# Performance work log

Measured on AMD Instinct MI355X. Metric: run time of the kernel, lower is better.

Reference implementation:

```python
import jax, jax.numpy as jnp
import numpy as np

STRIDES = (8, 4, 2, 1)
EPS = 1e-12  # F.normalize default eps


def _l2norm(x):
    return x / jnp.maximum(jnp.linalg.norm(x, axis=-1, keepdims=True), EPS)


def _stage(residual, stride, iw, ib, ow, ob, cb):
    B, D, T = residual.shape
    # avg_pool1d(stride, stride)
    zp = residual.reshape(B, D, T // stride, stride).mean(-1) if stride > 1 else residual
    # in_proj: 1x1 conv  [B,D,Ts] -> [B,C,Ts]
    z_e = jnp.einsum('bdt,cd->bct', zp, iw) + ib[None, :, None]
    C = z_e.shape[1]
    enc = z_e.transpose(0, 2, 1).reshape(-1, C)           # (B*Ts, C)
    enc_n = _l2norm(enc)
    cb_n = _l2norm(cb)
    dist = (enc_n ** 2).sum(1, keepdims=True) - 2.0 * enc_n @ cb_n.T + (cb_n ** 2).sum(1)[None, :]
    indices = jnp.argmax(-dist, axis=1).reshape(B, -1)    # (B, Ts)
    z_q = cb[indices].transpose(0, 2, 1)                  # (B, C, Ts) -- unnormalized codebook lookup
    commit = ((z_e - jax.lax.stop_gradient(z_q)) ** 2).mean(axis=(1, 2))
    cbloss = ((z_q - jax.lax.stop_gradient(z_e)) ** 2).mean(axis=(1, 2))
    z_q = z_e + jax.lax.stop_gradient(z_q - z_e)          # straight-through
    z_q_out = jnp.einsum('bct,dc->bdt', z_q, ow) + ob[None, :, None]
    if stride > 1:
        z_q_out = jnp.repeat(z_q_out, stride, axis=-1)
        z_e = jnp.repeat(z_e, stride, axis=-1)
    return z_q_out, commit, cbloss, indices, z_e


def setup_inputs() -> dict:
    key = jax.random.key(0)
    ks = jax.random.split(key, 6)
    return {
        'z': jax.random.normal(ks[0], (16, 512, 4096), dtype=jnp.float32),
        'in_w': jax.random.normal(ks[1], (4, 8, 512), dtype=jnp.float32) * 0.05,
        'in_b': jax.random.normal(ks[2], (4, 8), dtype=jnp.float32) * 0.05,
        'out_w': jax.random.normal(ks[3], (4, 512, 8), dtype=jnp.float32) * 0.05,
        'out_b': jax.random.normal(ks[4], (4, 512), dtype=jnp.float32) * 0.05,
        'codebooks': jax.random.normal(ks[5], (4, 1024, 8), dtype=jnp.float32),
    }


def reference(z, in_w, in_b, out_w, out_b, codebooks):
    z_q = jnp.zeros_like(z)
    residual = z
    commitment_loss = 0.0
    codebook_loss = 0.0
    codes = []
    latents = []
    for i, s in enumerate(STRIDES):
        z_q_i, commit_i, cbloss_i, idx_i, z_e_i = _stage(
            residual, s, in_w[i], in_b[i], out_w[i], out_b[i], codebooks[i])
        z_q = z_q + z_q_i  # mask is all-True in eval with n_quantizers = n_codebooks
        residual = residual - z_q_i
        commitment_loss = commitment_loss + commit_i.mean()
        codebook_loss = codebook_loss + cbloss_i.mean()
        codes.append(idx_i)
        latents.append(z_e_i)
    latents = jnp.concatenate(latents, axis=1)  # [B, N*C, T]
    return (z_q, latents, commitment_loss, codebook_loss,
            codes[0], codes[1], codes[2], codes[3])
```

## Files before the change

### kernel.cpp

```cpp
#include <hip/hip_runtime.h>


constexpr int B = 16, D = 512, T = 4096, C = 8, K = 1024, NS = 4;

constexpr long long OUT_ZQ     = 0;
constexpr long long OUT_LAT    = 33554432LL;
constexpr long long OUT_COMMIT = OUT_LAT + 2097152LL;
constexpr long long OUT_CBL    = OUT_COMMIT + 1;
constexpr long long OUT_CODES0 = OUT_CBL + 1;

__host__ __device__ constexpr long long code_off(int j) {
    return OUT_CODES0 + (j >= 1 ? 8192 : 0) + (j >= 2 ? 16384 : 0) + (j >= 3 ? 32768 : 0);
}

constexpr long long WS_CBREC = 0;
constexpr long long WS_OBS   = 49152;
constexpr long long WS_LOSS  = 49664;
constexpr long long WS_CORR  = 49696;
constexpr long long WS_P0    = 52224;
constexpr long long WS_P1    = WS_P0 + 65536;
constexpr long long WS_P2    = WS_P1 + 131072;
constexpr long long WS_P3    = WS_P2 + 262144;
constexpr long long WS_Q0    = WS_P3 + 524288;
constexpr long long WS_Q1    = WS_Q0 + 65536;
constexpr long long WS_Q2    = WS_Q1 + 131072;
constexpr long long WS_Q3    = WS_Q2 + 262144;
constexpr long long WS_TAB   = WS_Q3 + 524288;

__global__ __launch_bounds__(256) void k_prep(
    const float* __restrict__ in_w, const float* __restrict__ out_w,
    const float* __restrict__ out_b, const float* __restrict__ cb,
    float* __restrict__ ws)
{
    int bid = blockIdx.x;
    int tid = threadIdx.x;

    if (bid < 18) {
        int t = bid * 256 + tid;
        if (t == 0) ws[WS_LOSS] = 0.f;
        if (t < NS * K) {
            const float* c = cb + (long long)t * 8;
            float cv[8];
#pragma unroll
            for (int k = 0; k < 8; k++) cv[k] = c[k];
            float n2 = 0.f;
#pragma unroll
            for (int k = 0; k < 8; k++) n2 += cv[k] * cv[k];
            float den = fmaxf(sqrtf(n2), 1e-12f);
            float cn[8];
#pragma unroll
            for (int k = 0; k < 8; k++) cn[k] = cv[k] / den;
            float cn2 = 0.f;
#pragma unroll
            for (int k = 0; k < 8; k++) cn2 += cn[k] * cn[k];
            float* r = ws + WS_CBREC + (long long)t * 12;
#pragma unroll
            for (int k = 0; k < 8; k++) r[k] = -2.0f * cn[k];
            r[8] = cn2; r[9] = 0.f; r[10] = 0.f; r[11] = 0.f;
        } else if (t < NS * K + D) {
            int d = t - NS * K;
            ws[WS_OBS + d] = out_b[d] + out_b[512 + d] + out_b[1024 + d] + out_b[1536 + d];
        }
        return;
    }

    int gw = (bid - 18) * 4 + (tid >> 6);
    int lane = tid & 63;
    if (gw >= 6 * 72) return;
    int p = gw / 72, idx = gw % 72;
    int i, j;
    if (p == 0) { i = 1; j = 0; }
    else if (p < 3) { i = 2; j = p - 1; }
    else { i = 3; j = p - 3; }

    double acc = 0.0;
    if (idx < 64) {
        int ci = idx >> 3, cc = idx & 7;
        const float* wi = in_w + (long long)(i * 8 + ci) * 512;
        const float* wo = out_w + (long long)j * 4096;
#pragma unroll
        for (int k = 0; k < 8; k++) {
            int d = lane + k * 64;
            acc += (double)wi[d] * (double)wo[d * 8 + cc];
        }
    } else {
        int ci = idx - 64;
        const float* wi = in_w + (long long)(i * 8 + ci) * 512;
        const float* bo = out_b + (long long)j * 512;
#pragma unroll
        for (int k = 0; k < 8; k++) {
            int d = lane + k * 64;
            acc += (double)wi[d] * (double)bo[d];
        }
    }
#pragma unroll
    for (int off = 32; off >= 1; off >>= 1) acc += __shfl_down(acc, off);
    if (lane == 0) ((double*)(ws + WS_CORR))[p * 72 + idx] = acc;
}

__global__ __launch_bounds__(256) void k_prep_c(
    const float* __restrict__ cb, float* __restrict__ ws)
{
    int t = blockIdx.x * 256 + threadIdx.x;
    if (t >= 6 * 1024) return;
    int p = t >> 10, code = t & 1023;
    int j = (p == 0) ? 0 : (p < 3) ? (p - 1) : (p - 3);
    const double* M = (const double*)(ws + WS_CORR) + p * 72;
    const float* q = cb + ((long long)j * K + code) * 8;
    float qv[8];
#pragma unroll
    for (int cc = 0; cc < 8; cc++) qv[cc] = q[cc];
    float* trow = ws + WS_TAB + (long long)t * 8;
#pragma unroll
    for (int c = 0; c < 8; c++) {
        double acc = M[64 + c];
#pragma unroll
        for (int cc = 0; cc < 8; cc++) acc += M[c * 8 + cc] * (double)qv[cc];
        trow[c] = (float)acc;
    }
}

__global__ __launch_bounds__(512) void k_pool_proj(
    const float* __restrict__ z, const float* __restrict__ in_w,
    const float* __restrict__ in_b, float* __restrict__ ws)
{
    __shared__ float smem[512 * 36];

    int tid = threadIdx.x;
    int lane = tid & 63;
    int wv = __builtin_amdgcn_readfirstlane(tid >> 6);
    int b = blockIdx.x;
    int t0 = blockIdx.y * 128;

#pragma unroll
    for (int sc = 0; sc < 32; ++sc)
        smem[tid * 36 + sc] = in_w[sc * 512 + tid];
    __syncthreads();

    const float* zrow = z + ((long long)b * D) * T + t0 + lane * 2;

    float a3[2][8] = {};
    float a2[8]    = {};
    float a1[8]    = {};
    float a0[8]    = {};

#pragma unroll 2
    for (int dd = 0; dd < 64; dd++) {
        int d = wv * 64 + dd;
        float2 v = *(const float2*)(zrow + (long long)d * T);
        const float* wrow = smem + d * 36;
        float w0[8], w1[8], w2[8], w3[8];
        *(float4*)&w0[0] = *(const float4*)(wrow + 0);
        *(float4*)&w0[4] = *(const float4*)(wrow + 4);
        *(float4*)&w1[0] = *(const float4*)(wrow + 8);
        *(float4*)&w1[4] = *(const float4*)(wrow + 12);
        *(float4*)&w2[0] = *(const float4*)(wrow + 16);
        *(float4*)&w2[4] = *(const float4*)(wrow + 20);
        *(float4*)&w3[0] = *(const float4*)(wrow + 24);
        *(float4*)&w3[4] = *(const float4*)(wrow + 28);

        float s2 = v.x + v.y;
#pragma unroll
        for (int c = 0; c < 8; c++) {
            a3[0][c] = fmaf(w3[c], v.x, a3[0][c]);
            a3[1][c] = fmaf(w3[c], v.y, a3[1][c]);
            a2[c]    = fmaf(w2[c], s2, a2[c]);
            a1[c]    = fmaf(w1[c], s2, a1[c]);
            a0[c]    = fmaf(w0[c], s2, a0[c]);
        }
    }

    __syncthreads();

    {
        float (*red)[16][64] = (float (*)[16][64])smem;
#pragma unroll
        for (int pos = 0; pos < 2; pos++)
#pragma unroll
            for (int c = 0; c < 8; c++)
                red[wv][pos * 8 + c][lane] = a3[pos][c];
        __syncthreads();
        for (int o = tid; o < 1024; o += 512) {
            int ln = o & 63, s = o >> 6;
            float sum = 0.f;
#pragma unroll
            for (int w = 0; w < 8; w++) sum += red[w][s][ln];
            int pos = s >> 3, c = s & 7;
            int tp = t0 + ln * 2 + pos;
            ws[WS_P3 + ((long long)b * 4096 + tp) * 8 + c] = sum + in_b[3 * 8 + c];
        }
        __syncthreads();
    }

    {
        float (*red)[24][64] = (float (*)[24][64])smem;
#pragma unroll
        for (int c = 0; c < 8; c++) {
            red[wv][c][lane]      = a2[c];
            red[wv][8 + c][lane]  = a1[c];
            red[wv][16 + c][lane] = a0[c];
        }
        __syncthreads();
        for (int o = tid; o < 1536; o += 512) {
            int ln = o & 63, s = o >> 6;
            if (s < 8) {
                int c = s;
                float sum = 0.f;
#pragma unroll
                for (int w = 0; w < 8; w++) sum += red[w][s][ln];
                int tp = (t0 >> 1) + ln;
                ws[WS_P2 + ((long long)b * 2048 + tp) * 8 + c] = sum * 0.5f + in_b[2 * 8 + c];
            } else if (s < 16) {
                if (ln >= 32) continue;
                int c = s - 8;
                float sum = 0.f;
#pragma unroll
                for (int w = 0; w < 8; w++) sum += red[w][s][2 * ln] + red[w][s][2 * ln + 1];
                int tp = (t0 >> 2) + ln;
                ws[WS_P1 + ((long long)b * 1024 + tp) * 8 + c] = sum * 0.25f + in_b[8 + c];
            } else {
                if (ln >= 16) continue;
                int c = s - 16;
                float sum = 0.f;
#pragma unroll
                for (int w = 0; w < 8; w++)
#pragma unroll
                    for (int k = 0; k < 4; k++) sum += red[w][s][4 * ln + k];
                int tp = (t0 >> 3) + ln;
                ws[WS_P0 + ((long long)b * 512 + tp) * 8 + c] = sum * 0.125f + in_b[c];
            }
        }
    }
}

template <int S>
__global__ __launch_bounds__(512) void k_vq(
    const float* __restrict__ cb, float* __restrict__ ws, float* __restrict__ out)
{
    constexpr int TS = 512 << S;
    constexpr long long PBASE = (S == 0) ? WS_P0 : (S == 1) ? WS_P1 : (S == 2) ? WS_P2 : WS_P3;
    constexpr long long QBASE = (S == 0) ? WS_Q0 : (S == 1) ? WS_Q1 : (S == 2) ? WS_Q2 : WS_Q3;
    constexpr int pbase = (S == 1) ? 0 : (S == 2) ? 1 : 3;
    constexpr float LW = 1.0f / (8.0f * (float)TS * (float)B);

    __shared__ float cbl[12288];
    __shared__ float sb[8][64];
    __shared__ unsigned short si[8][64];
    __shared__ float e_lds[64][8];

    int tid = threadIdx.x;
    int lane = tid & 63;
    int w = __builtin_amdgcn_readfirstlane(tid >> 6);

    {
        const float4* src = (const float4*)(ws + WS_CBREC + (long long)S * K * 12);
        float4* dst = (float4*)cbl;
        for (int o = tid; o < 3072; o += 512) dst[o] = src[o];
    }

    long long v = (long long)blockIdx.x * 64 + lane;
    int b = (int)(v >> (9 + S));
    int tp = (int)(v & (TS - 1));

    float e[8];
    const float* P = ws + PBASE + v * 8;
#pragma unroll
    for (int c = 0; c < 8; c++) e[c] = P[c];

    if (S > 0) {
        double ed[8];
#pragma unroll
        for (int c = 0; c < 8; c++) ed[c] = (double)e[c];
#pragma unroll
        for (int j = 0; j < S; j++) {
            int tj = tp >> (S - j);
            long long vj = ((long long)b << (9 + j)) + tj;
            int cidx = (int)out[code_off(j) + vj];
            const float* trow = ws + WS_TAB + ((long long)(pbase + j) * 1024 + cidx) * 8;
#pragma unroll
            for (int c = 0; c < 8; c++) ed[c] -= (double)trow[c];
        }
#pragma unroll
        for (int c = 0; c < 8; c++) e[c] = (float)ed[c];
    }

    float n2 = 0.f;
#pragma unroll
    for (int c = 0; c < 8; c++) n2 = fmaf(e[c], e[c], n2);
    float den = fmaxf(sqrtf(n2), 1e-12f);
    float inv = 1.0f / den;
    float en[8];
#pragma unroll
    for (int c = 0; c < 8; c++) en[c] = e[c] * inv;

    if (w == 0) {
#pragma unroll
        for (int c = 0; c < 8; c++) e_lds[lane][c] = e[c];
    }

    __syncthreads();

    const float* rec = cbl + w * 128 * 12;
    float best = 3.0e38f;
    int bidx = 0;
    for (int jt = 0; jt < 128; jt++) {
        const float* r = rec + jt * 12;
        float acc = r[8];
#pragma unroll
        for (int c = 0; c < 8; c++) acc = fmaf(r[c], en[c], acc);
        if (acc < best) { best = acc; bidx = jt; }
    }
    sb[w][lane] = best;
    si[w][lane] = (unsigned short)(w * 128 + bidx);
    __syncthreads();

    if (tid < 64) {
        float bd = sb[0][lane];
        int bj = si[0][lane];
#pragma unroll
        for (int ww = 1; ww < 8; ww++) {
            float d2 = sb[ww][lane];
            int j2 = si[ww][lane];
            if (d2 < bd || (d2 == bd && j2 < bj)) { bd = d2; bj = j2; }
        }
        const float* qc = cb + ((long long)S * K + bj) * 8;
        float qv[8];
#pragma unroll
        for (int c = 0; c < 8; c++) qv[c] = qc[c];
        float* qo = ws + QBASE + v * 8;
#pragma unroll
        for (int c = 0; c < 8; c++) qo[c] = qv[c];

        out[code_off(S) + v] = (float)bj;

        float l = 0.f;
#pragma unroll
        for (int c = 0; c < 8; c++) { float dq = e[c] - qv[c]; l = fmaf(dq, dq, l); }
#pragma unroll
        for (int off = 32; off >= 1; off >>= 1) l += __shfl_down(l, off);
        if (lane == 0) atomicAdd(ws + WS_LOSS, l * LW);
    }

    constexpr int SREP = 8 >> S;
    {
        long long v0 = (long long)blockIdx.x * 64;
        int b0 = (int)(v0 >> (9 + S));
        int tp0 = (int)(v0 & (TS - 1));
        long long lat0 = OUT_LAT + ((long long)b0 * 32 + S * 8) * T + (long long)tp0 * SREP;
        for (int o = tid; o < 512 * SREP; o += 512) {
            int c = o / (64 * SREP);
            int r = o & (64 * SREP - 1);
            out[lat0 + (long long)c * T + r] = e_lds[r / SREP][c];
        }
    }
}

__global__ __launch_bounds__(256) void k_zq(
    const float* __restrict__ out_w, const float* __restrict__ ws, float* __restrict__ out)
{
    int tid = threadIdx.x;
    int lane = tid & 63;
    int w = __builtin_amdgcn_readfirstlane(tid >> 6);
    int bid = blockIdx.x;
    int tc   = bid & 3;
    int g    = (bid >> 2) & 63;
    int b    = bid >> 8;
    int t    = tc * 1024 + w * 256 + lane * 4;

    float q0[8], q1[8], q2[2][8], q3[4][8];
    {
        const float* Q = ws + WS_Q0 + ((long long)b * 512 + (t >> 3)) * 8;
#pragma unroll
        for (int c = 0; c < 8; c++) q0[c] = Q[c];
    }
    {
        const float* Q = ws + WS_Q1 + ((long long)b * 1024 + (t >> 2)) * 8;
#pragma unroll
        for (int c = 0; c < 8; c++) q1[c] = Q[c];
    }
    {
        const float* Q = ws + WS_Q2 + ((long long)b * 2048 + (t >> 1)) * 8;
#pragma unroll
        for (int j = 0; j < 2; j++)
#pragma unroll
            for (int c = 0; c < 8; c++) q2[j][c] = Q[j * 8 + c];
    }
    {
        const float* Q = ws + WS_Q3 + ((long long)b * 4096 + t) * 8;
#pragma unroll
        for (int j = 0; j < 4; j++)
#pragma unroll
            for (int c = 0; c < 8; c++) q3[j][c] = Q[j * 8 + c];
    }

#pragma unroll 2
    for (int dl = 0; dl < 8; dl++) {
        int d = g * 8 + dl;
        const float* w0 = out_w + 0 * 4096 + d * 8;
        const float* w1 = out_w + 1 * 4096 + d * 8;
        const float* w2 = out_w + 2 * 4096 + d * 8;
        const float* w3 = out_w + 3 * 4096 + d * 8;

        float acc = ws[WS_OBS + d];
#pragma unroll
        for (int c = 0; c < 8; c++) acc = fmaf(w0[c], q0[c], acc);
#pragma unroll
        for (int c = 0; c < 8; c++) acc = fmaf(w1[c], q1[c], acc);
        float accA = acc, accB = acc;
#pragma unroll
        for (int c = 0; c < 8; c++) {
            accA = fmaf(w2[c], q2[0][c], accA);
            accB = fmaf(w2[c], q2[1][c], accB);
        }
        float r0 = accA, r1 = accA, r2 = accB, r3 = accB;
#pragma unroll
        for (int c = 0; c < 8; c++) {
            r0 = fmaf(w3[c], q3[0][c], r0);
            r1 = fmaf(w3[c], q3[1][c], r1);
            r2 = fmaf(w3[c], q3[2][c], r2);
            r3 = fmaf(w3[c], q3[3][c], r3);
        }
        float* o = out + OUT_ZQ + ((long long)b * 512 + d) * T + t;
        *(float4*)o = make_float4(r0, r1, r2, r3);
    }

    if (bid == 0 && tid == 0) {
        float L = ws[WS_LOSS];
        out[OUT_COMMIT] = L;
        out[OUT_CBL]    = L;
    }
}

extern "C" void kernel_launch(void* const* d_in, const int* in_sizes, int n_in,
                              void* d_out, int out_size, void* d_ws, size_t ws_size,
                              hipStream_t stream)
{
    const float* z     = (const float*)d_in[0];
    const float* in_w  = (const float*)d_in[1];
    const float* in_b  = (const float*)d_in[2];
    const float* out_w = (const float*)d_in[3];
    const float* out_b = (const float*)d_in[4];
    const float* cb    = (const float*)d_in[5];
    float* out = (float*)d_out;
    float* ws  = (float*)d_ws;

    k_prep<<<dim3(126), dim3(256), 0, stream>>>(in_w, out_w, out_b, cb, ws);
    k_prep_c<<<dim3(24), dim3(256), 0, stream>>>(cb, ws);
    k_pool_proj<<<dim3(16, 32), dim3(512), 0, stream>>>(z, in_w, in_b, ws);
    k_vq<0><<<dim3(128), dim3(512), 0, stream>>>(cb, ws, out);
    k_vq<1><<<dim3(256), dim3(512), 0, stream>>>(cb, ws, out);
    k_vq<2><<<dim3(512), dim3(512), 0, stream>>>(cb, ws, out);
    k_vq<3><<<dim3(1024), dim3(512), 0, stream>>>(cb, ws, out);
    k_zq<<<dim3(4096), dim3(256), 0, stream>>>(out_w, ws, out);
}
```

Before: 151.1 us.

## Split VQ search across codebook chunks with atomicMin packed keys

Replaces the per-stage monolithic VQ kernel with three steps: one kernel computes the residual latent and writes the latents output, one scans codebook chunks in parallel over a 2D grid with four vectors per thread, and one emits the codes and losses. Partial argmins are merged through 64-bit atomicMin on keys that pack an order-preserving float distance with the code index. Quantized vectors are no longer stored but gathered from the codebook in k_zq. The aim is more parallelism for the small early stages and more register reuse per codebook row, at the cost of extra launches, key initialisation and global atomics.

```diff
diff --git a/kernel.cpp b/kernel.cpp
--- a/kernel.cpp
+++ b/kernel.cpp
@@ -14,18 +14,23 @@
 }
 
 constexpr long long WS_CBREC = 0;
-constexpr long long WS_OBS   = 49152;
-constexpr long long WS_LOSS  = 49664;
-constexpr long long WS_CORR  = 49696;
-constexpr long long WS_P0    = 52224;
+constexpr long long WS_CN2   = 32768;
+constexpr long long WS_OBS   = 36864;
+constexpr long long WS_LOSS  = 37376;
+constexpr long long WS_CORR  = 37384;
+constexpr long long WS_P0    = 40960;
 constexpr long long WS_P1    = WS_P0 + 65536;
 constexpr long long WS_P2    = WS_P1 + 131072;
 constexpr long long WS_P3    = WS_P2 + 262144;
-constexpr long long WS_Q0    = WS_P3 + 524288;
-constexpr long long WS_Q1    = WS_Q0 + 65536;
-constexpr long long WS_Q2    = WS_Q1 + 131072;
-constexpr long long WS_Q3    = WS_Q2 + 262144;
-constexpr long long WS_TAB   = WS_Q3 + 524288;
+constexpr long long WS_TAB   = WS_P3 + 524288;
+constexpr long long WS_KEY   = WS_TAB + 49152;
+
+__host__ __device__ constexpr long long key_off(int s) {
+    return (s >= 1 ? 8192 : 0) + (s >= 2 ? 16384 : 0) + (s >= 3 ? 32768 : 0);
+}
+__host__ __device__ constexpr long long pbase_of(int s) {
+    return (s == 0) ? WS_P0 : (s == 1) ? WS_P1 : (s == 2) ? WS_P2 : WS_P3;
+}
 
 __global__ __launch_bounds__(256) void k_prep(
     const float* __restrict__ in_w, const float* __restrict__ out_w,
@@ -52,11 +57,11 @@
             for (int k = 0; k < 8; k++) cn[k] = cv[k] / den;
             float cn2 = 0.f;
 #pragma unroll
-            for (int k = 0; k < 8; k++) cn2 += cn[k] * cn[k];
-            float* r = ws + WS_CBREC + (long long)t * 12;
+            for (int k = 0; k < 8; k++) cn2 = fmaf(cn[k], cn[k], cn2);
+            float* r = ws + WS_CBREC + (long long)t * 8;
 #pragma unroll
             for (int k = 0; k < 8; k++) r[k] = -2.0f * cn[k];
-            r[8] = cn2; r[9] = 0.f; r[10] = 0.f; r[11] = 0.f;
+            ws[WS_CN2 + t] = cn2;
         } else if (t < NS * K + D) {
             int d = t - NS * K;
             ws[WS_OBS + d] = out_b[d] + out_b[512 + d] + out_b[1024 + d] + out_b[1536 + d];
@@ -101,22 +106,31 @@
 __global__ __launch_bounds__(256) void k_prep_c(
     const float* __restrict__ cb, float* __restrict__ ws)
 {
-    int t = blockIdx.x * 256 + threadIdx.x;
-    if (t >= 6 * 1024) return;
-    int p = t >> 10, code = t & 1023;
-    int j = (p == 0) ? 0 : (p < 3) ? (p - 1) : (p - 3);
-    const double* M = (const double*)(ws + WS_CORR) + p * 72;
-    const float* q = cb + ((long long)j * K + code) * 8;
-    float qv[8];
-#pragma unroll
-    for (int cc = 0; cc < 8; cc++) qv[cc] = q[cc];
-    float* trow = ws + WS_TAB + (long long)t * 8;
-#pragma unroll
-    for (int c = 0; c < 8; c++) {
-        double acc = M[64 + c];
-#pragma unroll
-        for (int cc = 0; cc < 8; cc++) acc += M[c * 8 + cc] * (double)qv[cc];
-        trow[c] = (float)acc;
+    int bid = blockIdx.x;
+    int tid = threadIdx.x;
+    if (bid < 24) {
+        int t = bid * 256 + tid;
+        if (t < 6 * 1024) {
+            int p = t >> 10, code = t & 1023;
+            int j = (p == 0) ? 0 : (p < 3) ? (p - 1) : (p - 3);
+            const double* M = (const double*)(ws + WS_CORR) + p * 72;
+            const float* q = cb + ((long long)j * K + code) * 8;
+            float qv[8];
+#pragma unroll
+            for (int cc = 0; cc < 8; cc++) qv[cc] = q[cc];
+            float* trow = ws + WS_TAB + (long long)t * 8;
+#pragma unroll
+            for (int c = 0; c < 8; c++) {
+                double acc = M[64 + c];
+#pragma unroll
+                for (int cc = 0; cc < 8; cc++) acc += M[c * 8 + cc] * (double)qv[cc];
+                trow[c] = (float)acc;
+            }
+        }
+    } else {
+        long long o = (long long)(bid - 24) * 256 + tid;
+        if (o < 122880)
+            ((unsigned long long*)(ws + WS_KEY))[o] = 0xFFFFFFFFFFFFFFFFULL;
     }
 }
 
@@ -234,129 +248,200 @@
 }
 
 template <int S>
-__global__ __launch_bounds__(512) void k_vq(
-    const float* __restrict__ cb, float* __restrict__ ws, float* __restrict__ out)
+__global__ __launch_bounds__(512) void k_en(
+    float* __restrict__ ws, float* __restrict__ out)
 {
     constexpr int TS = 512 << S;
-    constexpr long long PBASE = (S == 0) ? WS_P0 : (S == 1) ? WS_P1 : (S == 2) ? WS_P2 : WS_P3;
-    constexpr long long QBASE = (S == 0) ? WS_Q0 : (S == 1) ? WS_Q1 : (S == 2) ? WS_Q2 : WS_Q3;
+    constexpr long long EBASE = pbase_of(S);
     constexpr int pbase = (S == 1) ? 0 : (S == 2) ? 1 : 3;
-    constexpr float LW = 1.0f / (8.0f * (float)TS * (float)B);
-
-    __shared__ float cbl[12288];
-    __shared__ float sb[8][64];
-    __shared__ unsigned short si[8][64];
-    __shared__ float e_lds[64][8];
+    constexpr int SREP = 8 >> S;
+
+    long long v = (long long)blockIdx.x * 512 + threadIdx.x;
+    int b = (int)(v >> (9 + S));
+    int tp = (int)(v & (TS - 1));
+
+    float e[8];
+    float* E = ws + EBASE + v * 8;
+    *(float4*)&e[0] = *(const float4*)(E + 0);
+    *(float4*)&e[4] = *(const float4*)(E + 4);
+
+    if constexpr (S > 0) {
+        const unsigned long long* keys = (const unsigned long long*)(ws + WS_KEY);
+        double ed[8];
+#pragma unroll
+        for (int c = 0; c < 8; c++) ed[c] = (double)e[c];
+#pragma unroll
+        for (int j = 0; j < S; j++) {
+            int tj = tp >> (S - j);
+            long long vj = ((long long)b << (9 + j)) + tj;
+            int cidx = (int)(unsigned)keys[key_off(j) + vj];
+            const float* trow = ws + WS_TAB + ((long long)(pbase + j) * 1024 + cidx) * 8;
+#pragma unroll
+            for (int c = 0; c < 8; c++) ed[c] -= (double)trow[c];
+        }
+#pragma unroll
+        for (int c = 0; c < 8; c++) e[c] = (float)ed[c];
+        *(float4*)(E + 0) = *(const float4*)&e[0];
+        *(float4*)(E + 4) = *(const float4*)&e[4];
+    }
+
+    long long lat0 = OUT_LAT + ((long long)b * 32 + S * 8) * T + (long long)tp * SREP;
+#pragma unroll
+    for (int c = 0; c < 8; c++) {
+        float* o = out + lat0 + (long long)c * T;
+        if constexpr (SREP == 8) {
+            float4 fv = make_float4(e[c], e[c], e[c], e[c]);
+            *(float4*)(o + 0) = fv;
+            *(float4*)(o + 4) = fv;
+        } else if constexpr (SREP == 4) {
+            *(float4*)o = make_float4(e[c], e[c], e[c], e[c]);
+        } else if constexpr (SREP == 2) {
+            *(float2*)o = make_float2(e[c], e[c]);
+        } else {
+            *o = e[c];
+        }
+    }
+}
+
+template <int S>
+__global__ __launch_bounds__(512) void k_scan(float* __restrict__ ws)
+{
+    constexpr int F = 8 >> S;
+    constexpr int CHUNK = 1024 / F;
+    constexpr int CPW = CHUNK / 8;
+    constexpr long long EBASE = pbase_of(S);
+
+    __shared__ float recl[CHUNK * 8];
+    __shared__ float cn2l[CHUNK];
+    __shared__ float sbl[8][256];
+    __shared__ unsigned short sil[8][256];
 
     int tid = threadIdx.x;
     int lane = tid & 63;
     int w = __builtin_amdgcn_readfirstlane(tid >> 6);
+    int ck = blockIdx.x;
+    int vb = blockIdx.y;
 
     {
-        const float4* src = (const float4*)(ws + WS_CBREC + (long long)S * K * 12);
-        float4* dst = (float4*)cbl;
-        for (int o = tid; o < 3072; o += 512) dst[o] = src[o];
-    }
-
-    long long v = (long long)blockIdx.x * 64 + lane;
-    int b = (int)(v >> (9 + S));
-    int tp = (int)(v & (TS - 1));
-
-    float e[8];
-    const float* P = ws + PBASE + v * 8;
-#pragma unroll
-    for (int c = 0; c < 8; c++) e[c] = P[c];
-
-    if (S > 0) {
-        double ed[8];
-#pragma unroll
-        for (int c = 0; c < 8; c++) ed[c] = (double)e[c];
-#pragma unroll
-        for (int j = 0; j < S; j++) {
-            int tj = tp >> (S - j);
-            long long vj = ((long long)b << (9 + j)) + tj;
-            int cidx = (int)out[code_off(j) + vj];
-            const float* trow = ws + WS_TAB + ((long long)(pbase + j) * 1024 + cidx) * 8;
-#pragma unroll
-            for (int c = 0; c < 8; c++) ed[c] -= (double)trow[c];
-        }
-#pragma unroll
-        for (int c = 0; c < 8; c++) e[c] = (float)ed[c];
-    }
-
-    float n2 = 0.f;
-#pragma unroll
-    for (int c = 0; c < 8; c++) n2 = fmaf(e[c], e[c], n2);
-    float den = fmaxf(sqrtf(n2), 1e-12f);
-    float inv = 1.0f / den;
-    float en[8];
-#pragma unroll
-    for (int c = 0; c < 8; c++) en[c] = e[c] * inv;
-
-    if (w == 0) {
-#pragma unroll
-        for (int c = 0; c < 8; c++) e_lds[lane][c] = e[c];
+        const float4* rs = (const float4*)(ws + WS_CBREC + (long long)S * 8192 + (long long)ck * CHUNK * 8);
+        float4* rd = (float4*)recl;
+        for (int o = tid; o < CHUNK * 2; o += 512) rd[o] = rs[o];
+        const float4* cs = (const float4*)(ws + WS_CN2 + (long long)S * 1024 + (long long)ck * CHUNK);
+        float4* cd = (float4*)cn2l;
+        for (int o = tid; o < CHUNK / 4; o += 512) cd[o] = cs[o];
+    }
+
+    float en[4][8];
+#pragma unroll
+    for (int h = 0; h < 4; h++) {
+        long long v = (long long)vb * 256 + h * 64 + lane;
+        const float* E = ws + EBASE + v * 8;
+        float e[8];
+        *(float4*)&e[0] = *(const float4*)(E + 0);
+        *(float4*)&e[4] = *(const float4*)(E + 4);
+        float n2 = 0.f;
+#pragma unroll
+        for (int c = 0; c < 8; c++) n2 = fmaf(e[c], e[c], n2);
+        float den = fmaxf(sqrtf(n2), 1e-12f);
+        float inv = 1.0f / den;
+#pragma unroll
+        for (int c = 0; c < 8; c++) en[h][c] = e[c] * inv;
     }
 
     __syncthreads();
 
-    const float* rec = cbl + w * 128 * 12;
-    float best = 3.0e38f;
-    int bidx = 0;
-    for (int jt = 0; jt < 128; jt++) {
-        const float* r = rec + jt * 12;
-        float acc = r[8];
-#pragma unroll
-        for (int c = 0; c < 8; c++) acc = fmaf(r[c], en[c], acc);
-        if (acc < best) { best = acc; bidx = jt; }
-    }
-    sb[w][lane] = best;
-    si[w][lane] = (unsigned short)(w * 128 + bidx);
+    const float* rec = recl + w * CPW * 8;
+    const float* c2  = cn2l + w * CPW;
+    float best0 = 3.0e38f, best1 = 3.0e38f, best2 = 3.0e38f, best3 = 3.0e38f;
+    int bi0 = 0, bi1 = 0, bi2 = 0, bi3 = 0;
+
+    for (int j0 = 0; j0 < CPW; j0 += 4) {
+        float4 cq = *(const float4*)(c2 + j0);
+        float cqa[4] = { cq.x, cq.y, cq.z, cq.w };
+#pragma unroll
+        for (int k = 0; k < 4; k++) {
+            int jt = j0 + k;
+            const float* r = rec + jt * 8;
+            float rr[8];
+            *(float4*)&rr[0] = *(const float4*)(r + 0);
+            *(float4*)&rr[4] = *(const float4*)(r + 4);
+            float cc = cqa[k];
+            float a0 = cc, a1 = cc, a2 = cc, a3 = cc;
+#pragma unroll
+            for (int c = 0; c < 8; c++) {
+                float rc = rr[c];
+                a0 = fmaf(rc, en[0][c], a0);
+                a1 = fmaf(rc, en[1][c], a1);
+                a2 = fmaf(rc, en[2][c], a2);
+                a3 = fmaf(rc, en[3][c], a3);
+            }
+            if (a0 < best0) { best0 = a0; bi0 = jt; }
+            if (a1 < best1) { best1 = a1; bi1 = jt; }
+            if (a2 < best2) { best2 = a2; bi2 = jt; }
+            if (a3 < best3) { best3 = a3; bi3 = jt; }
+        }
+    }
+
+    sbl[w][lane]       = best0;  sil[w][lane]       = (unsigned short)(w * CPW + bi0);
+    sbl[w][64 + lane]  = best1;  sil[w][64 + lane]  = (unsigned short)(w * CPW + bi1);
+    sbl[w][128 + lane] = best2;  sil[w][128 + lane] = (unsigned short)(w * CPW + bi2);
+    sbl[w][192 + lane] = best3;  sil[w][192 + lane] = (unsigned short)(w * CPW + bi3);
     __syncthreads();
 
-    if (tid < 64) {
-        float bd = sb[0][lane];
-        int bj = si[0][lane];
+    if (tid < 256) {
+        int sv = tid;
+        float bd = sbl[0][sv];
+        int bj = sil[0][sv];
 #pragma unroll
         for (int ww = 1; ww < 8; ww++) {
-            float d2 = sb[ww][lane];
-            int j2 = si[ww][lane];
+            float d2 = sbl[ww][sv];
+            int j2 = sil[ww][sv];
             if (d2 < bd || (d2 == bd && j2 < bj)) { bd = d2; bj = j2; }
         }
-        const float* qc = cb + ((long long)S * K + bj) * 8;
-        float qv[8];
-#pragma unroll
-        for (int c = 0; c < 8; c++) qv[c] = qc[c];
-        float* qo = ws + QBASE + v * 8;
-#pragma unroll
-        for (int c = 0; c < 8; c++) qo[c] = qv[c];
-
-        out[code_off(S) + v] = (float)bj;
-
-        float l = 0.f;
-#pragma unroll
-        for (int c = 0; c < 8; c++) { float dq = e[c] - qv[c]; l = fmaf(dq, dq, l); }
-#pragma unroll
-        for (int off = 32; off >= 1; off >>= 1) l += __shfl_down(l, off);
-        if (lane == 0) atomicAdd(ws + WS_LOSS, l * LW);
-    }
-
-    constexpr int SREP = 8 >> S;
-    {
-        long long v0 = (long long)blockIdx.x * 64;
-        int b0 = (int)(v0 >> (9 + S));
-        int tp0 = (int)(v0 & (TS - 1));
-        long long lat0 = OUT_LAT + ((long long)b0 * 32 + S * 8) * T + (long long)tp0 * SREP;
-        for (int o = tid; o < 512 * SREP; o += 512) {
-            int c = o / (64 * SREP);
-            int r = o & (64 * SREP - 1);
-            out[lat0 + (long long)c * T + r] = e_lds[r / SREP][c];
-        }
-    }
+        int code = ck * CHUNK + bj;
+        unsigned u = __float_as_uint(bd);
+        u = (u & 0x80000000u) ? ~u : (u | 0x80000000u);
+        unsigned long long key = ((unsigned long long)u << 32) | (unsigned)code;
+        long long v = (long long)vb * 256 + sv;
+        atomicMin((unsigned long long*)(ws + WS_KEY) + key_off(S) + v, key);
+    }
+}
+
+__global__ __launch_bounds__(256) void k_emit(
+    const float* __restrict__ cb, float* __restrict__ ws, float* __restrict__ out)
+{
+    int bid = blockIdx.x;
+    int tid = threadIdx.x;
+    long long t = (long long)bid * 256 + tid;
+
+    int S = (t < 8192) ? 0 : (t < 24576) ? 1 : (t < 57344) ? 2 : 3;
+    long long base = (S == 0) ? 0 : (S == 1) ? 8192 : (S == 2) ? 24576 : 57344;
+    long long v = t - base;
+    long long ebase = (S == 0) ? WS_P0 : (S == 1) ? WS_P1 : (S == 2) ? WS_P2 : WS_P3;
+
+    unsigned long long key = ((const unsigned long long*)(ws + WS_KEY))[base + v];
+    int bj = (int)(unsigned)key;
+
+    out[code_off(S) + v] = (float)bj;
+
+    const float* E = ws + ebase + v * 8;
+    const float* qc = cb + ((long long)S * K + bj) * 8;
+    float l = 0.f;
+#pragma unroll
+    for (int c = 0; c < 8; c++) {
+        float dq = E[c] - qc[c];
+        l = fmaf(dq, dq, l);
+    }
+    float LW = 1.0f / (float)(65536 << S);
+    l *= LW;
+#pragma unroll
+    for (int off = 32; off >= 1; off >>= 1) l += __shfl_down(l, off);
+    if ((tid & 63) == 0) atomicAdd(ws + WS_LOSS, l);
 }
 
 __global__ __launch_bounds__(256) void k_zq(
-    const float* __restrict__ out_w, const float* __restrict__ ws, float* __restrict__ out)
+    const float* __restrict__ out_w, const float* __restrict__ cb,
+    const float* __restrict__ ws, float* __restrict__ out)
 {
     int tid = threadIdx.x;
     int lane = tid & 63;
@@ -367,30 +452,34 @@
     int b    = bid >> 8;
     int t    = tc * 1024 + w * 256 + lane * 4;
 
+    const unsigned long long* keys = (const unsigned long long*)(ws + WS_KEY);
+
     float q0[8], q1[8], q2[2][8], q3[4][8];
     {
-        const float* Q = ws + WS_Q0 + ((long long)b * 512 + (t >> 3)) * 8;
+        int bj = (int)(unsigned)keys[key_off(0) + (long long)b * 512 + (t >> 3)];
+        const float* Q = cb + (long long)bj * 8;
 #pragma unroll
         for (int c = 0; c < 8; c++) q0[c] = Q[c];
     }
     {
-        const float* Q = ws + WS_Q1 + ((long long)b * 1024 + (t >> 2)) * 8;
+        int bj = (int)(unsigned)keys[key_off(1) + (long long)b * 1024 + (t >> 2)];
+        const float* Q = cb + (long long)(K + bj) * 8;
 #pragma unroll
         for (int c = 0; c < 8; c++) q1[c] = Q[c];
     }
-    {
-        const float* Q = ws + WS_Q2 + ((long long)b * 2048 + (t >> 1)) * 8;
-#pragma unroll
-        for (int j = 0; j < 2; j++)
-#pragma unroll
-            for (int c = 0; c < 8; c++) q2[j][c] = Q[j * 8 + c];
-    }
-    {
-        const float* Q = ws + WS_Q3 + ((long long)b * 4096 + t) * 8;
-#pragma unroll
-        for (int j = 0; j < 4; j++)
-#pragma unroll
-            for (int c = 0; c < 8; c++) q3[j][c] = Q[j * 8 + c];
+#pragma unroll
+    for (int j = 0; j < 2; j++) {
+        int bj = (int)(unsigned)keys[key_off(2) + (long long)b * 2048 + (t >> 1) + j];
+        const float* Q = cb + (long long)(2 * K + bj) * 8;
+#pragma unroll
+        for (int c = 0; c < 8; c++) q2[j][c] = Q[c];
+    }
+#pragma unroll
+    for (int j = 0; j < 4; j++) {
+        int bj = (int)(unsigned)keys[key_off(3) + (long long)b * 4096 + t + j];
+        const float* Q = cb + (long long)(3 * K + bj) * 8;
+#pragma unroll
+        for (int c = 0; c < 8; c++) q3[j][c] = Q[c];
     }
 
 #pragma unroll 2
@@ -445,11 +534,18 @@
     float* ws  = (float*)d_ws;
 
     k_prep<<<dim3(126), dim3(256), 0, stream>>>(in_w, out_w, out_b, cb, ws);
-    k_prep_c<<<dim3(24), dim3(256), 0, stream>>>(cb, ws);
+    k_prep_c<<<dim3(504), dim3(256), 0, stream>>>(cb, ws);
     k_pool_proj<<<dim3(16, 32), dim3(512), 0, stream>>>(z, in_w, in_b, ws);
-    k_vq<0><<<dim3(128), dim3(512), 0, stream>>>(cb, ws, out);
-    k_vq<1><<<dim3(256), dim3(512), 0, stream>>>(cb, ws, out);
-    k_vq<2><<<dim3(512), dim3(512), 0, stream>>>(cb, ws, out);
-    k_vq<3><<<dim3(1024), dim3(512), 0, stream>>>(cb, ws, out);
-    k_zq<<<dim3(4096), dim3(256), 0, stream>>>(out_w, ws, out);
-}
+
+    k_en<0><<<dim3(16), dim3(512), 0, stream>>>(ws, out);
+    k_scan<0><<<dim3(8, 32), dim3(512), 0, stream>>>(ws);
+    k_en<1><<<dim3(32), dim3(512), 0, stream>>>(ws, out);
+    k_scan<1><<<dim3(4, 64), dim3(512), 0, stream>>>(ws);
+    k_en<2><<<dim3(64), dim3(512), 0, stream>>>(ws, out);
+    k_scan<2><<<dim3(2, 128), dim3(512), 0, stream>>>(ws);
+    k_en<3><<<dim3(128), dim3(512), 0, stream>>>(ws, out);
+    k_scan<3><<<dim3(1, 256), dim3(512), 0, stream>>>(ws);
+
+    k_emit<<<dim3(480), dim3(256), 0, stream>>>(cb, ws, out);
+    k_zq<<<dim3(4096), dim3(256), 0, stream>>>(out_w, cb, ws, out);
+}
```

New measurement: 164.9 us. +9.1%, slower.
